# Performance work log

Hardware: AMD Instinct MI355X
Metric: run time of the kernel (lower is better)

Reference implementation:

```python
import jax, jax.numpy as jnp
import numpy as np

B, H, S, D = 2, 12, 2048, 64

def setup_inputs() -> dict:
    key = jax.random.key(0)
    kq, kk, kv = jax.random.split(key, 3)
    Q = jax.random.normal(kq, (B, H, S, D), dtype=jnp.float32)
    K = jax.random.normal(kk, (B, H, S, D), dtype=jnp.float32)
    V = jax.random.normal(kv, (B, H, S, D), dtype=jnp.float32)
    return {"Q": Q, "K": K, "V": V}

def reference(Q, K, V):
    # NOTE: original code scales by sqrt(Q.shape[-2]) (the sequence length),
    # not the head dim — reproduced faithfully.
    scale = 1.0 / np.sqrt(Q.shape[-2]).astype(np.float32)
    scores = jnp.einsum('bhqd,bhkd->bhqk', Q, K) * scale  # [B,H,S,S]
    attn = jax.nn.softmax(scores, axis=-1)
    context = jnp.einsum('bhqk,bhkd->bhqd', attn, V)      # [B,H,S,D]
    # torch .squeeze(-1) only removes the last dim if it is size 1; D=64 so no-op
    return context
```

## Files before the change

kernel.cpp:

```cpp
#include <hip/hip_runtime.h>
#include <hip/hip_bf16.h>
#include <math.h>
#include <stdint.h>

#define BATCH 2
#define NH 12
#define SEQ 2048
#define HD 64
#define TQ 64
#define TK 64
#define NHEADS (BATCH*NH)
#define NIT (SEQ / TK)

typedef short bf16x8 __attribute__((ext_vector_type(8)));
typedef float f32x4 __attribute__((ext_vector_type(4)));
typedef float f32x16 __attribute__((ext_vector_type(16)));
typedef unsigned short us4_t __attribute__((ext_vector_type(4)));
typedef unsigned short us8_t __attribute__((ext_vector_type(8)));

#if __has_builtin(__builtin_amdgcn_exp2f)
#define EXP2F(x) __builtin_amdgcn_exp2f(x)
#else
#define EXP2F(x) exp2f(x)
#endif

static __device__ __forceinline__ unsigned short f2bf(float f) {
    unsigned int u = __float_as_uint(f);
    u += 0x7fffu + ((u >> 16) & 1u);
    return (unsigned short)(u >> 16);
}

static __device__ __forceinline__ unsigned int pack2bf(float a, float b) {
    __hip_bfloat162 v = __float22bfloat162_rn(float2{a, b});
    return *(unsigned int*)&v;
}

static __device__ __forceinline__ void async_cp16(const void* g, void* l) {
    __builtin_amdgcn_global_load_lds(
        (const __attribute__((address_space(1))) void*)g,
        (__attribute__((address_space(3))) void*)(uintptr_t)l,
        16, 0, 0);
}

static __device__ __forceinline__ int tile_off(int r, int c) {
    int rp  = r >> 1;
    int pos = (((r & 1) << 3) | c) ^ (rp & 15);
    return rp * 128 + pos * 8;
}

__global__ __launch_bounds__(256)
void prep_kv(const float* __restrict__ K, const float* __restrict__ V,
             unsigned short* __restrict__ Kb, unsigned short* __restrict__ Vtb) {
    __shared__ unsigned short T[64][66];
    const int bh = blockIdx.x >> 5;
    const int s0 = (blockIdx.x & 31) * 64;
    const int tid = threadIdx.x;
    const size_t off = ((size_t)bh * SEQ + s0) * HD;

    #pragma unroll
    for (int u = 0; u < 4; ++u) {
        int idx = u * 1024 + tid * 4;
        float4 a = *(const float4*)&K[off + idx];
        us4_t r4 = { f2bf(a.x), f2bf(a.y), f2bf(a.z), f2bf(a.w) };
        *(us4_t*)&Kb[off + idx] = r4;
    }
    #pragma unroll
    for (int u = 0; u < 4; ++u) {
        int idx = u * 1024 + tid * 4;
        int r = idx >> 6, col = idx & 63;
        float4 a = *(const float4*)&V[off + idx];
        *(unsigned int*)&T[r][col]     = pack2bf(a.x, a.y);
        *(unsigned int*)&T[r][col + 2] = pack2bf(a.z, a.w);
    }
    __syncthreads();
    unsigned short* Vdst = Vtb + (size_t)bh * HD * SEQ;
    const int g = tid & 7, dd = tid >> 3;
    #pragma unroll
    for (int h = 0; h < 2; ++h) {
        int d = dd + 32 * h;
        us8_t r8;
        #pragma unroll
        for (int j = 0; j < 8; ++j) r8[j] = T[g * 8 + j][d];
        *(us8_t*)&Vdst[(size_t)d * SEQ + s0 + g * 8] = r8;
    }
}

__global__ __launch_bounds__(256)
void fa_main(const float* __restrict__ Q,
             const unsigned short* __restrict__ Kb,
             const unsigned short* __restrict__ Vtb,
             float* __restrict__ O, float qs) {
    const int x  = blockIdx.x & 7;
    const int t  = blockIdx.x >> 3;
    const int bh = x + 8 * (t % 3);
    const int qt = t / 3;
    const int q0 = qt * TQ;

    __shared__ __align__(16) unsigned short KtS[2][4096];
    __shared__ __align__(16) unsigned short VtS[2][4096];
    __shared__ __align__(16) unsigned short Ps[4096];
    __shared__ float Lsum[64];
    __shared__ float Linv[64];

    const int tid  = threadIdx.x;
    const int w    = tid >> 6;
    const int mt   = w >> 1;
    const int nt   = w & 1;
    const int lane = tid & 63;
    const int l31  = lane & 31;
    const int hi   = lane >> 5;

    const float*          Qh = Q   + ((size_t)bh * SEQ + q0) * HD;
    const unsigned short* Kh = Kb  + (size_t)bh * SEQ * HD;
    const unsigned short* Vh = Vtb + (size_t)bh * HD * SEQ;

    int rS[2], cS[2];
    #pragma unroll
    for (int i = 0; i < 2; ++i) {
        int rp = w * 8 + 4 * i + (lane >> 4);
        int lc = (lane & 15) ^ (rp & 15);
        rS[i] = 2 * rp + (lc >> 3);
        cS[i] = lc & 7;
    }
    const int dst0 = (w * 8 + 0) * 128, dst1 = (w * 8 + 4) * 128;
    const size_t kG0 = (size_t)rS[0] * HD  + cS[0] * 8;
    const size_t kG1 = (size_t)rS[1] * HD  + cS[1] * 8;
    const size_t vG0 = (size_t)rS[0] * SEQ + cS[0] * 8;
    const size_t vG1 = (size_t)rS[1] * SEQ + cS[1] * 8;

    async_cp16(Kh + kG0, &KtS[0][dst0]);
    async_cp16(Kh + kG1, &KtS[0][dst1]);
    async_cp16(Vh + vG0, &VtS[0][dst0]);
    async_cp16(Vh + vG1, &VtS[0][dst1]);
    #pragma unroll
    for (int u = 0; u < 4; ++u) {
        int idx = u * 1024 + tid * 4;
        int r = idx >> 6, col = idx & 63;
        float4 a = *(const float4*)&Qh[idx];
        uint2 pk = { pack2bf(a.x * qs, a.y * qs), pack2bf(a.z * qs, a.w * qs) };
        *(uint2*)&Ps[tile_off(r, col >> 3) + (col & 7)] = pk;
    }
    __syncthreads();

    bf16x8 qf[4];
    #pragma unroll
    for (int s = 0; s < 4; ++s)
        qf[s] = *(const bf16x8*)&Ps[tile_off(mt * 32 + l31, s * 2 + hi)];
    __syncthreads();

    const int m = mt * 32 + l31;
    int kOffL[4], vOffL[2][2], pW[4], pR[2];
    #pragma unroll
    for (int s = 0; s < 4; ++s) kOffL[s] = tile_off(nt * 32 + l31, s * 2 + hi);
    #pragma unroll
    for (int dt = 0; dt < 2; ++dt)
        #pragma unroll
        for (int ks = 0; ks < 2; ++ks)
            vOffL[dt][ks] = tile_off(dt * 32 + l31, nt * 4 + ks * 2 + hi);
    #pragma unroll
    for (int g = 0; g < 4; ++g) pW[g] = tile_off(m, nt * 4 + g) + hi * 4;
    #pragma unroll
    for (int ks = 0; ks < 2; ++ks) pR[ks] = tile_off(m, nt * 4 + ks * 2 + hi);

    f32x16 o[2];
    o[0] = (f32x16)(0.f);
    o[1] = (f32x16)(0.f);
    float lsum = 0.f;

    for (int it = 0; it < NIT; ++it) {
        const int cur = it & 1;
        if (it + 1 < NIT) {
            const int nb = cur ^ 1;
            const size_t kv = (size_t)(it + 1) * TK;
            async_cp16(Kh + kv * HD + kG0, &KtS[nb][dst0]);
            async_cp16(Kh + kv * HD + kG1, &KtS[nb][dst1]);
            async_cp16(Vh + kv + vG0,      &VtS[nb][dst0]);
            async_cp16(Vh + kv + vG1,      &VtS[nb][dst1]);
        }
        const unsigned short* Ks = KtS[cur];
        const unsigned short* Vs = VtS[cur];

        f32x16 sc = (f32x16)(0.f);
        #pragma unroll
        for (int s = 0; s < 4; ++s) {
            bf16x8 kf = *(const bf16x8*)&Ks[kOffL[s]];
            sc = __builtin_amdgcn_mfma_f32_32x32x16_bf16(kf, qf[s], sc, 0, 0, 0);
        }

        #pragma unroll
        for (int g = 0; g < 4; ++g) {
            float p0 = EXP2F(sc[4*g+0]);
            float p1 = EXP2F(sc[4*g+1]);
            float p2 = EXP2F(sc[4*g+2]);
            float p3 = EXP2F(sc[4*g+3]);
            lsum += (p0 + p1) + (p2 + p3);
            uint2 pk = { pack2bf(p0, p1), pack2bf(p2, p3) };
            *(uint2*)&Ps[pW[g]] = pk;
        }

        bf16x8 pf0 = *(const bf16x8*)&Ps[pR[0]];
        bf16x8 pf1 = *(const bf16x8*)&Ps[pR[1]];
        #pragma unroll
        for (int dt = 0; dt < 2; ++dt) {
            bf16x8 vf0 = *(const bf16x8*)&Vs[vOffL[dt][0]];
            o[dt] = __builtin_amdgcn_mfma_f32_32x32x16_bf16(pf0, vf0, o[dt], 0, 0, 0);
            bf16x8 vf1 = *(const bf16x8*)&Vs[vOffL[dt][1]];
            o[dt] = __builtin_amdgcn_mfma_f32_32x32x16_bf16(pf1, vf1, o[dt], 0, 0, 0);
        }

        __syncthreads();
    }

    lsum += __shfl_xor(lsum, 32, 64);
    float* ORed = (float*)&KtS[0][0];

    if (nt == 1) {
        if (lane < 32) Lsum[mt * 32 + lane] = lsum;
        #pragma unroll
        for (int dt = 0; dt < 2; ++dt) {
            const int d = dt * 32 + l31;
            #pragma unroll
            for (int g = 0; g < 4; ++g) {
                const int m0 = mt * 32 + 8 * g + 4 * hi;
                const int ph = (m0 >> 2) ^ (d & 15);
                float4 v = { o[dt][4*g+0], o[dt][4*g+1], o[dt][4*g+2], o[dt][4*g+3] };
                *(float4*)&ORed[d * 64 + ph * 4] = v;
            }
        }
    }
    __syncthreads();

    if (nt == 0) {
        float ltot = lsum + Lsum[mt * 32 + l31];
        if (lane < 32) Linv[mt * 32 + lane] = 1.0f / ltot;
        float* Oh = O + ((size_t)bh * SEQ + q0) * HD;
        #pragma unroll
        for (int dt = 0; dt < 2; ++dt) {
            const int d = dt * 32 + l31;
            #pragma unroll
            for (int g = 0; g < 4; ++g) {
                const int m0 = mt * 32 + 8 * g + 4 * hi;
                const int ph = (m0 >> 2) ^ (d & 15);
                float4 part = *(const float4*)&ORed[d * 64 + ph * 4];
                float4 inv4 = *(const float4*)&Linv[m0];
                const float* pp = (const float*)&part;
                const float* ii = (const float*)&inv4;
                #pragma unroll
                for (int j = 0; j < 4; ++j)
                    Oh[(size_t)(m0 + j) * HD + d] = (o[dt][4*g+j] + pp[j]) * ii[j];
            }
        }
    }
}

#define PAD 8
#define LSTR (HD + PAD)

__global__ __launch_bounds__(256)
void fa_fwd_fb(const float* __restrict__ Q, const float* __restrict__ K,
               const float* __restrict__ V, float* __restrict__ O) {
    const int x  = blockIdx.x & 7;
    const int t  = blockIdx.x >> 3;
    const int bh = x + 8 * (t % 3);
    const int qt = t / 3;
    const int q0 = qt * TQ;
    const long base = (long)bh * SEQ * HD;

    __shared__ unsigned short Qs[TQ][LSTR];
    __shared__ unsigned short Ks2[TK][LSTR];
    __shared__ unsigned short Vt[HD][TK + PAD];
    __shared__ unsigned short Ps2[4][16][LSTR];

    const int tid  = threadIdx.x;
    const int wave = tid >> 6;
    const int lane = tid & 63;
    const int col  = lane & 15;
    const int quad = lane >> 4;
    const int m0   = wave * 16;

    #pragma unroll
    for (int i = 0; i < 4; ++i) {
        int idx = tid + 256 * i;
        int row = idx >> 4;
        int c4  = (idx & 15) * 4;
        float4 v = *(const float4*)&Q[base + (long)(q0 + row) * HD + c4];
        ushort4 b = { f2bf(v.x), f2bf(v.y), f2bf(v.z), f2bf(v.w) };
        *(ushort4*)&Qs[row][c4] = b;
    }
    __syncthreads();

    bf16x8 aq0 = *(const bf16x8*)&Qs[m0 + col][quad * 8];
    bf16x8 aq1 = *(const bf16x8*)&Qs[m0 + col][32 + quad * 8];

    f32x4 o0 = {0.f,0.f,0.f,0.f}, o1 = o0, o2 = o0, o3 = o0;
    float l[4] = {0.f, 0.f, 0.f, 0.f};
    const float scale = 0.022097086912079608f;

    for (int kv0 = 0; kv0 < SEQ; kv0 += TK) {
        __syncthreads();
        #pragma unroll
        for (int i = 0; i < 4; ++i) {
            int idx = tid + 256 * i;
            int row = idx >> 4;
            int c4  = (idx & 15) * 4;
            float4 kv = *(const float4*)&K[base + (long)(kv0 + row) * HD + c4];
            ushort4 kb = { f2bf(kv.x), f2bf(kv.y), f2bf(kv.z), f2bf(kv.w) };
            *(ushort4*)&Ks2[row][c4] = kb;
            float4 vv = *(const float4*)&V[base + (long)(kv0 + row) * HD + c4];
            Vt[c4 + 0][row] = f2bf(vv.x);
            Vt[c4 + 1][row] = f2bf(vv.y);
            Vt[c4 + 2][row] = f2bf(vv.z);
            Vt[c4 + 3][row] = f2bf(vv.w);
        }
        __syncthreads();

        f32x4 sc[4];
        #pragma unroll
        for (int n = 0; n < 4; ++n) {
            bf16x8 b0 = *(const bf16x8*)&Ks2[n * 16 + col][quad * 8];
            bf16x8 b1 = *(const bf16x8*)&Ks2[n * 16 + col][32 + quad * 8];
            f32x4 acc = {0.f,0.f,0.f,0.f};
            acc = __builtin_amdgcn_mfma_f32_16x16x32_bf16(aq0, b0, acc, 0, 0, 0);
            acc = __builtin_amdgcn_mfma_f32_16x16x32_bf16(aq1, b1, acc, 0, 0, 0);
            sc[n] = acc;
        }

        float tsum[4] = {0.f, 0.f, 0.f, 0.f};
        #pragma unroll
        for (int n = 0; n < 4; ++n) {
            #pragma unroll
            for (int r = 0; r < 4; ++r) {
                float p = __expf(sc[n][r] * scale);
                tsum[r] += p;
                Ps2[wave][quad * 4 + r][n * 16 + col] = f2bf(p);
            }
        }
        #pragma unroll
        for (int off = 1; off < 16; off <<= 1) {
            #pragma unroll
            for (int r = 0; r < 4; ++r) tsum[r] += __shfl_xor(tsum[r], off, 64);
        }
        #pragma unroll
        for (int r = 0; r < 4; ++r) l[r] += tsum[r];

        bf16x8 ap0 = *(const bf16x8*)&Ps2[wave][col][quad * 8];
        bf16x8 ap1 = *(const bf16x8*)&Ps2[wave][col][32 + quad * 8];
        #pragma unroll
        for (int n = 0; n < 4; ++n) {
            bf16x8 b0 = *(const bf16x8*)&Vt[n * 16 + col][quad * 8];
            bf16x8 b1 = *(const bf16x8*)&Vt[n * 16 + col][32 + quad * 8];
            f32x4* op = (n == 0) ? &o0 : (n == 1) ? &o1 : (n == 2) ? &o2 : &o3;
            *op = __builtin_amdgcn_mfma_f32_16x16x32_bf16(ap0, b0, *op, 0, 0, 0);
            *op = __builtin_amdgcn_mfma_f32_16x16x32_bf16(ap1, b1, *op, 0, 0, 0);
        }
    }

    float inv[4];
    #pragma unroll
    for (int r = 0; r < 4; ++r) inv[r] = 1.0f / l[r];
    #pragma unroll
    for (int r = 0; r < 4; ++r) {
        long row = base + (long)(q0 + m0 + quad * 4 + r) * HD;
        O[row +  0 + col] = o0[r] * inv[r];
        O[row + 16 + col] = o1[r] * inv[r];
        O[row + 32 + col] = o2[r] * inv[r];
        O[row + 48 + col] = o3[r] * inv[r];
    }
}

extern "C" void kernel_launch(void* const* d_in, const int* in_sizes, int n_in,
                              void* d_out, int out_size, void* d_ws, size_t ws_size,
                              hipStream_t stream) {
    const float* Q = (const float*)d_in[0];
    const float* K = (const float*)d_in[1];
    const float* V = (const float*)d_in[2];
    float* O = (float*)d_out;

    const size_t tensorElems = (size_t)NHEADS * SEQ * HD;
    const size_t need = 2 * tensorElems * sizeof(unsigned short);

    if (ws_size >= need) {
        unsigned short* Kb  = (unsigned short*)d_ws;
        unsigned short* Vtb = Kb + tensorElems;
        const float qs = (float)(1.4426950408889634 / sqrt(2048.0));
        prep_kv<<<dim3(NHEADS * (SEQ / 64)), dim3(256), 0, stream>>>(K, V, Kb, Vtb);
        fa_main<<<dim3(NHEADS * (SEQ / TQ)), dim3(256), 0, stream>>>(Q, Kb, Vtb, O, qs);
    } else {
        fa_fwd_fb<<<dim3(NHEADS * (SEQ / TQ)), dim3(256), 0, stream>>>(Q, K, V, O);
    }
}
```

Measured before the change: 125.6 us.

## Split KV across waves with register-resident K/V fragments and LDS reduction

Each wave now owns a 32-key slice of a 128-key block and loads its K and V fragments straight from global memory into registers, prefetching the next block one iteration ahead. This replaces the shared-memory double buffer and the per-iteration block barrier. Every wave computes all 64 query rows, so partial outputs and row sums are combined across the four waves through shared memory at the end. The intent is to remove LDS staging traffic and the barriers from the main loop, at the cost of higher register pressure, a serialized four-step reduction, and less coalesced direct global loads.

```diff
diff --git a/kernel.cpp b/kernel.cpp
--- a/kernel.cpp
+++ b/kernel.cpp
@@ -8,9 +8,9 @@
 #define SEQ 2048
 #define HD 64
 #define TQ 64
-#define TK 64
+#define TKK 128
 #define NHEADS (BATCH*NH)
-#define NIT (SEQ / TK)
+#define NITK (SEQ / TKK)
 
 typedef short bf16x8 __attribute__((ext_vector_type(8)));
 typedef float f32x4 __attribute__((ext_vector_type(4)));
@@ -35,17 +35,15 @@
     return *(unsigned int*)&v;
 }
 
-static __device__ __forceinline__ void async_cp16(const void* g, void* l) {
-    __builtin_amdgcn_global_load_lds(
-        (const __attribute__((address_space(1))) void*)g,
-        (__attribute__((address_space(3))) void*)(uintptr_t)l,
-        16, 0, 0);
-}
-
 static __device__ __forceinline__ int tile_off(int r, int c) {
     int rp  = r >> 1;
     int pos = (((r & 1) << 3) | c) ^ (rp & 15);
     return rp * 128 + pos * 8;
+}
+static __device__ __forceinline__ int poff32(int r, int c) {
+    int rp  = r >> 1;
+    int pos = (((r & 1) << 2) | c) ^ (rp & 7);
+    return rp * 64 + pos * 8;
 }
 
 __global__ __launch_bounds__(256)
@@ -96,16 +94,13 @@
     const int qt = t / 3;
     const int q0 = qt * TQ;
 
-    __shared__ __align__(16) unsigned short KtS[2][4096];
-    __shared__ __align__(16) unsigned short VtS[2][4096];
-    __shared__ __align__(16) unsigned short Ps[4096];
-    __shared__ float Lsum[64];
-    __shared__ float Linv[64];
+    __shared__ __align__(16) unsigned char SHraw[18432];
+    unsigned short* Qst   = (unsigned short*)SHraw;
+    float*          ORed  = (float*)SHraw;
+    float*          Lpart = (float*)(SHraw + 17408);
 
     const int tid  = threadIdx.x;
     const int w    = tid >> 6;
-    const int mt   = w >> 1;
-    const int nt   = w & 1;
     const int lane = tid & 63;
     const int l31  = lane & 31;
     const int hi   = lane >> 5;
@@ -114,142 +109,146 @@
     const unsigned short* Kh = Kb  + (size_t)bh * SEQ * HD;
     const unsigned short* Vh = Vtb + (size_t)bh * HD * SEQ;
 
-    int rS[2], cS[2];
-    #pragma unroll
-    for (int i = 0; i < 2; ++i) {
-        int rp = w * 8 + 4 * i + (lane >> 4);
-        int lc = (lane & 15) ^ (rp & 15);
-        rS[i] = 2 * rp + (lc >> 3);
-        cS[i] = lc & 7;
-    }
-    const int dst0 = (w * 8 + 0) * 128, dst1 = (w * 8 + 4) * 128;
-    const size_t kG0 = (size_t)rS[0] * HD  + cS[0] * 8;
-    const size_t kG1 = (size_t)rS[1] * HD  + cS[1] * 8;
-    const size_t vG0 = (size_t)rS[0] * SEQ + cS[0] * 8;
-    const size_t vG1 = (size_t)rS[1] * SEQ + cS[1] * 8;
-
-    async_cp16(Kh + kG0, &KtS[0][dst0]);
-    async_cp16(Kh + kG1, &KtS[0][dst1]);
-    async_cp16(Vh + vG0, &VtS[0][dst0]);
-    async_cp16(Vh + vG1, &VtS[0][dst1]);
+    const unsigned short* Kq = Kh + (size_t)(w * 32 + l31) * HD + hi * 8;
+    const unsigned short* Vq = Vh + (size_t)l31 * SEQ + w * 32 + hi * 8;
+
+    us8_t kc[4], vc[4];
+    #pragma unroll
+    for (int s = 0; s < 4; ++s) kc[s] = *(const us8_t*)&Kq[s * 16];
+    #pragma unroll
+    for (int dt = 0; dt < 2; ++dt)
+        #pragma unroll
+        for (int ks = 0; ks < 2; ++ks)
+            vc[dt * 2 + ks] = *(const us8_t*)&Vq[(size_t)dt * 32 * SEQ + ks * 16];
+
     #pragma unroll
     for (int u = 0; u < 4; ++u) {
         int idx = u * 1024 + tid * 4;
         int r = idx >> 6, col = idx & 63;
         float4 a = *(const float4*)&Qh[idx];
         uint2 pk = { pack2bf(a.x * qs, a.y * qs), pack2bf(a.z * qs, a.w * qs) };
-        *(uint2*)&Ps[tile_off(r, col >> 3) + (col & 7)] = pk;
-    }
-    __syncthreads();
-
-    bf16x8 qf[4];
-    #pragma unroll
-    for (int s = 0; s < 4; ++s)
-        qf[s] = *(const bf16x8*)&Ps[tile_off(mt * 32 + l31, s * 2 + hi)];
-    __syncthreads();
-
-    const int m = mt * 32 + l31;
-    int kOffL[4], vOffL[2][2], pW[4], pR[2];
-    #pragma unroll
-    for (int s = 0; s < 4; ++s) kOffL[s] = tile_off(nt * 32 + l31, s * 2 + hi);
-    #pragma unroll
-    for (int dt = 0; dt < 2; ++dt)
-        #pragma unroll
-        for (int ks = 0; ks < 2; ++ks)
-            vOffL[dt][ks] = tile_off(dt * 32 + l31, nt * 4 + ks * 2 + hi);
-    #pragma unroll
-    for (int g = 0; g < 4; ++g) pW[g] = tile_off(m, nt * 4 + g) + hi * 4;
-    #pragma unroll
-    for (int ks = 0; ks < 2; ++ks) pR[ks] = tile_off(m, nt * 4 + ks * 2 + hi);
-
-    f32x16 o[2];
-    o[0] = (f32x16)(0.f);
-    o[1] = (f32x16)(0.f);
-    float lsum = 0.f;
-
-    for (int it = 0; it < NIT; ++it) {
-        const int cur = it & 1;
-        if (it + 1 < NIT) {
-            const int nb = cur ^ 1;
-            const size_t kv = (size_t)(it + 1) * TK;
-            async_cp16(Kh + kv * HD + kG0, &KtS[nb][dst0]);
-            async_cp16(Kh + kv * HD + kG1, &KtS[nb][dst1]);
-            async_cp16(Vh + kv + vG0,      &VtS[nb][dst0]);
-            async_cp16(Vh + kv + vG1,      &VtS[nb][dst1]);
-        }
-        const unsigned short* Ks = KtS[cur];
-        const unsigned short* Vs = VtS[cur];
-
-        f32x16 sc = (f32x16)(0.f);
+        *(uint2*)&Qst[tile_off(r, col >> 3) + (col & 7)] = pk;
+    }
+    __syncthreads();
+    bf16x8 qf[2][4];
+    #pragma unroll
+    for (int mt = 0; mt < 2; ++mt)
+        #pragma unroll
+        for (int s = 0; s < 4; ++s)
+            qf[mt][s] = *(const bf16x8*)&Qst[tile_off(mt * 32 + l31, s * 2 + hi)];
+    __syncthreads();
+
+    unsigned short* Psw = (unsigned short*)SHraw + w * 2048;
+
+    int pWo[2][4], pRo[2][2];
+    #pragma unroll
+    for (int mt = 0; mt < 2; ++mt) {
+        #pragma unroll
+        for (int g = 0; g < 4; ++g)  pWo[mt][g]  = poff32(mt * 32 + l31, g) + hi * 4;
+        #pragma unroll
+        for (int ks = 0; ks < 2; ++ks) pRo[mt][ks] = poff32(mt * 32 + l31, ks * 2 + hi);
+    }
+
+    f32x16 o[2][2];
+    o[0][0] = (f32x16)(0.f); o[0][1] = (f32x16)(0.f);
+    o[1][0] = (f32x16)(0.f); o[1][1] = (f32x16)(0.f);
+    float lsum[2] = {0.f, 0.f};
+
+    #pragma unroll 2
+    for (int it = 0; it < NITK; ++it) {
+        us8_t kn[4], vn[4];
+        if (it + 1 < NITK) {
+            const size_t ko = (size_t)(it + 1) * TKK * HD;
+            const size_t vo = (size_t)(it + 1) * TKK;
+            #pragma unroll
+            for (int s = 0; s < 4; ++s) kn[s] = *(const us8_t*)&Kq[ko + s * 16];
+            #pragma unroll
+            for (int dt = 0; dt < 2; ++dt)
+                #pragma unroll
+                for (int ks = 0; ks < 2; ++ks)
+                    vn[dt * 2 + ks] = *(const us8_t*)&Vq[vo + (size_t)dt * 32 * SEQ + ks * 16];
+        }
+
+        f32x16 sc0 = (f32x16)(0.f), sc1 = (f32x16)(0.f);
         #pragma unroll
         for (int s = 0; s < 4; ++s) {
-            bf16x8 kf = *(const bf16x8*)&Ks[kOffL[s]];
-            sc = __builtin_amdgcn_mfma_f32_32x32x16_bf16(kf, qf[s], sc, 0, 0, 0);
-        }
-
-        #pragma unroll
-        for (int g = 0; g < 4; ++g) {
-            float p0 = EXP2F(sc[4*g+0]);
-            float p1 = EXP2F(sc[4*g+1]);
-            float p2 = EXP2F(sc[4*g+2]);
-            float p3 = EXP2F(sc[4*g+3]);
-            lsum += (p0 + p1) + (p2 + p3);
-            uint2 pk = { pack2bf(p0, p1), pack2bf(p2, p3) };
-            *(uint2*)&Ps[pW[g]] = pk;
-        }
-
-        bf16x8 pf0 = *(const bf16x8*)&Ps[pR[0]];
-        bf16x8 pf1 = *(const bf16x8*)&Ps[pR[1]];
-        #pragma unroll
-        for (int dt = 0; dt < 2; ++dt) {
-            bf16x8 vf0 = *(const bf16x8*)&Vs[vOffL[dt][0]];
-            o[dt] = __builtin_amdgcn_mfma_f32_32x32x16_bf16(pf0, vf0, o[dt], 0, 0, 0);
-            bf16x8 vf1 = *(const bf16x8*)&Vs[vOffL[dt][1]];
-            o[dt] = __builtin_amdgcn_mfma_f32_32x32x16_bf16(pf1, vf1, o[dt], 0, 0, 0);
-        }
-
+            bf16x8 kf = (bf16x8)kc[s];
+            sc0 = __builtin_amdgcn_mfma_f32_32x32x16_bf16(kf, qf[0][s], sc0, 0, 0, 0);
+            sc1 = __builtin_amdgcn_mfma_f32_32x32x16_bf16(kf, qf[1][s], sc1, 0, 0, 0);
+        }
+
+        #pragma unroll
+        for (int mt = 0; mt < 2; ++mt) {
+            const f32x16 s = mt ? sc1 : sc0;
+            #pragma unroll
+            for (int g = 0; g < 4; ++g) {
+                float p0 = EXP2F(s[4*g+0]);
+                float p1 = EXP2F(s[4*g+1]);
+                float p2 = EXP2F(s[4*g+2]);
+                float p3 = EXP2F(s[4*g+3]);
+                lsum[mt] += (p0 + p1) + (p2 + p3);
+                uint2 pk = { pack2bf(p0, p1), pack2bf(p2, p3) };
+                *(uint2*)&Psw[pWo[mt][g]] = pk;
+            }
+        }
+
+        bf16x8 pf[2][2];
+        #pragma unroll
+        for (int mt = 0; mt < 2; ++mt)
+            #pragma unroll
+            for (int ks = 0; ks < 2; ++ks)
+                pf[mt][ks] = *(const bf16x8*)&Psw[pRo[mt][ks]];
+        #pragma unroll
+        for (int dt = 0; dt < 2; ++dt)
+            #pragma unroll
+            for (int ks = 0; ks < 2; ++ks) {
+                bf16x8 vf = (bf16x8)vc[dt * 2 + ks];
+                o[0][dt] = __builtin_amdgcn_mfma_f32_32x32x16_bf16(pf[0][ks], vf, o[0][dt], 0, 0, 0);
+                o[1][dt] = __builtin_amdgcn_mfma_f32_32x32x16_bf16(pf[1][ks], vf, o[1][dt], 0, 0, 0);
+            }
+
+        #pragma unroll
+        for (int s = 0; s < 4; ++s) { kc[s] = kn[s]; vc[s] = vn[s]; }
+    }
+
+    #pragma unroll
+    for (int mt = 0; mt < 2; ++mt) lsum[mt] += __shfl_xor(lsum[mt], 32, 64);
+    if (lane < 32) {
+        Lpart[w * 64 + l31]      = lsum[0];
+        Lpart[w * 64 + 32 + l31] = lsum[1];
+    }
+
+    #pragma unroll
+    for (int rr = 0; rr < 4; ++rr) {
         __syncthreads();
-    }
-
-    lsum += __shfl_xor(lsum, 32, 64);
-    float* ORed = (float*)&KtS[0][0];
-
-    if (nt == 1) {
-        if (lane < 32) Lsum[mt * 32 + lane] = lsum;
-        #pragma unroll
-        for (int dt = 0; dt < 2; ++dt) {
-            const int d = dt * 32 + l31;
-            #pragma unroll
-            for (int g = 0; g < 4; ++g) {
-                const int m0 = mt * 32 + 8 * g + 4 * hi;
-                const int ph = (m0 >> 2) ^ (d & 15);
-                float4 v = { o[dt][4*g+0], o[dt][4*g+1], o[dt][4*g+2], o[dt][4*g+3] };
-                *(float4*)&ORed[d * 64 + ph * 4] = v;
-            }
-        }
-    }
-    __syncthreads();
-
-    if (nt == 0) {
-        float ltot = lsum + Lsum[mt * 32 + l31];
-        if (lane < 32) Linv[mt * 32 + lane] = 1.0f / ltot;
-        float* Oh = O + ((size_t)bh * SEQ + q0) * HD;
-        #pragma unroll
-        for (int dt = 0; dt < 2; ++dt) {
-            const int d = dt * 32 + l31;
-            #pragma unroll
-            for (int g = 0; g < 4; ++g) {
-                const int m0 = mt * 32 + 8 * g + 4 * hi;
-                const int ph = (m0 >> 2) ^ (d & 15);
-                float4 part = *(const float4*)&ORed[d * 64 + ph * 4];
-                float4 inv4 = *(const float4*)&Linv[m0];
-                const float* pp = (const float*)&part;
-                const float* ii = (const float*)&inv4;
+        if (w == rr) {
+            #pragma unroll
+            for (int mt = 0; mt < 2; ++mt)
                 #pragma unroll
-                for (int j = 0; j < 4; ++j)
-                    Oh[(size_t)(m0 + j) * HD + d] = (o[dt][4*g+j] + pp[j]) * ii[j];
-            }
-        }
+                for (int dt = 0; dt < 2; ++dt) {
+                    const int d = dt * 32 + l31;
+                    #pragma unroll
+                    for (int g = 0; g < 4; ++g) {
+                        const int m0 = mt * 32 + 8 * g + 4 * hi;
+                        float4 v = { o[mt][dt][4*g+0], o[mt][dt][4*g+1],
+                                     o[mt][dt][4*g+2], o[mt][dt][4*g+3] };
+                        if (rr != 0) {
+                            float4 p = *(const float4*)&ORed[d * 68 + m0];
+                            v.x += p.x; v.y += p.y; v.z += p.z; v.w += p.w;
+                        }
+                        *(float4*)&ORed[d * 68 + m0] = v;
+                    }
+                }
+        }
+    }
+    __syncthreads();
+
+    float* Oh = O + ((size_t)bh * SEQ + q0) * HD;
+    #pragma unroll
+    for (int i = 0; i < 16; ++i) {
+        const int m = w * 16 + i;
+        float ltot = Lpart[m] + Lpart[64 + m] + Lpart[128 + m] + Lpart[192 + m];
+        Oh[(size_t)m * HD + lane] = ORed[lane * 68 + m] * (1.0f / ltot);
     }
 }
 
@@ -267,8 +266,8 @@
     const long base = (long)bh * SEQ * HD;
 
     __shared__ unsigned short Qs[TQ][LSTR];
-    __shared__ unsigned short Ks2[TK][LSTR];
-    __shared__ unsigned short Vt[HD][TK + PAD];
+    __shared__ unsigned short Ks2[64][LSTR];
+    __shared__ unsigned short Vt[HD][64 + PAD];
     __shared__ unsigned short Ps2[4][16][LSTR];
 
     const int tid  = threadIdx.x;
@@ -296,7 +295,7 @@
     float l[4] = {0.f, 0.f, 0.f, 0.f};
     const float scale = 0.022097086912079608f;
 
-    for (int kv0 = 0; kv0 < SEQ; kv0 += TK) {
+    for (int kv0 = 0; kv0 < SEQ; kv0 += 64) {
         __syncthreads();
         #pragma unroll
         for (int i = 0; i < 4; ++i) {
```

Measured after the change: 135.7 us. +8.1%, slower.

## Keep softmax probabilities in registers by permuting V layout, drop P shared buffer

Applied to the files above, without the earlier changes.

The V-transpose prep kernel now writes keys in a permuted order that matches the MFMA accumulator layout. This lets the exponentiated scores be packed straight into bf16 B-operand registers for the PV product, with no round-trip through a shared-memory P tile. Shared memory is merged into one raw buffer with the Q staging reusing a V buffer, occupancy is hinted with launch_bounds(256,4), and V fragments are loaded before the QK MFMAs to hide LDS latency. The risk is that a mismatch between the register layout and the key permutation would silently give wrong results.

```diff
diff --git a/kernel.cpp b/kernel.cpp
--- a/kernel.cpp
+++ b/kernel.cpp
@@ -17,6 +17,7 @@
 typedef float f32x16 __attribute__((ext_vector_type(16)));
 typedef unsigned short us4_t __attribute__((ext_vector_type(4)));
 typedef unsigned short us8_t __attribute__((ext_vector_type(8)));
+typedef unsigned int u32x4 __attribute__((ext_vector_type(4)));
 
 #if __has_builtin(__builtin_amdgcn_exp2f)
 #define EXP2F(x) __builtin_amdgcn_exp2f(x)
@@ -80,12 +81,15 @@
         int d = dd + 32 * h;
         us8_t r8;
         #pragma unroll
-        for (int j = 0; j < 8; ++j) r8[j] = T[g * 8 + j][d];
+        for (int j = 0; j < 8; ++j) {
+            int src = ((g >> 1) << 4) + ((j >> 2) << 3) + ((g & 1) << 2) + (j & 3);
+            r8[j] = T[src][d];
+        }
         *(us8_t*)&Vdst[(size_t)d * SEQ + s0 + g * 8] = r8;
     }
 }
 
-__global__ __launch_bounds__(256)
+__global__ __launch_bounds__(256, 4)
 void fa_main(const float* __restrict__ Q,
              const unsigned short* __restrict__ Kb,
              const unsigned short* __restrict__ Vtb,
@@ -96,11 +100,14 @@
     const int qt = t / 3;
     const int q0 = qt * TQ;
 
-    __shared__ __align__(16) unsigned short KtS[2][4096];
-    __shared__ __align__(16) unsigned short VtS[2][4096];
-    __shared__ __align__(16) unsigned short Ps[4096];
-    __shared__ float Lsum[64];
-    __shared__ float Linv[64];
+    __shared__ __align__(16) unsigned char SH[33280];
+    unsigned short* Ksh0 = (unsigned short*)SH;
+    unsigned short* Ksh1 = (unsigned short*)(SH + 8192);
+    unsigned short* Vsh0 = (unsigned short*)(SH + 16384);
+    unsigned short* Vsh1 = (unsigned short*)(SH + 24576);
+    float* Lsum = (float*)(SH + 32768);
+    float* Linv = (float*)(SH + 33024);
+    float* ORed = (float*)SH;
 
     const int tid  = threadIdx.x;
     const int w    = tid >> 6;
@@ -128,28 +135,27 @@
     const size_t vG0 = (size_t)rS[0] * SEQ + cS[0] * 8;
     const size_t vG1 = (size_t)rS[1] * SEQ + cS[1] * 8;
 
-    async_cp16(Kh + kG0, &KtS[0][dst0]);
-    async_cp16(Kh + kG1, &KtS[0][dst1]);
-    async_cp16(Vh + vG0, &VtS[0][dst0]);
-    async_cp16(Vh + vG1, &VtS[0][dst1]);
+    async_cp16(Kh + kG0, &Ksh0[dst0]);
+    async_cp16(Kh + kG1, &Ksh0[dst1]);
+    async_cp16(Vh + vG0, &Vsh0[dst0]);
+    async_cp16(Vh + vG1, &Vsh0[dst1]);
     #pragma unroll
     for (int u = 0; u < 4; ++u) {
         int idx = u * 1024 + tid * 4;
         int r = idx >> 6, col = idx & 63;
         float4 a = *(const float4*)&Qh[idx];
         uint2 pk = { pack2bf(a.x * qs, a.y * qs), pack2bf(a.z * qs, a.w * qs) };
-        *(uint2*)&Ps[tile_off(r, col >> 3) + (col & 7)] = pk;
+        *(uint2*)&Vsh1[tile_off(r, col >> 3) + (col & 7)] = pk;
     }
     __syncthreads();
 
     bf16x8 qf[4];
     #pragma unroll
     for (int s = 0; s < 4; ++s)
-        qf[s] = *(const bf16x8*)&Ps[tile_off(mt * 32 + l31, s * 2 + hi)];
-    __syncthreads();
-
-    const int m = mt * 32 + l31;
-    int kOffL[4], vOffL[2][2], pW[4], pR[2];
+        qf[s] = *(const bf16x8*)&Vsh1[tile_off(mt * 32 + l31, s * 2 + hi)];
+    __syncthreads();
+
+    int kOffL[4], vOffL[2][2];
     #pragma unroll
     for (int s = 0; s < 4; ++s) kOffL[s] = tile_off(nt * 32 + l31, s * 2 + hi);
     #pragma unroll
@@ -157,28 +163,33 @@
         #pragma unroll
         for (int ks = 0; ks < 2; ++ks)
             vOffL[dt][ks] = tile_off(dt * 32 + l31, nt * 4 + ks * 2 + hi);
-    #pragma unroll
-    for (int g = 0; g < 4; ++g) pW[g] = tile_off(m, nt * 4 + g) + hi * 4;
-    #pragma unroll
-    for (int ks = 0; ks < 2; ++ks) pR[ks] = tile_off(m, nt * 4 + ks * 2 + hi);
 
     f32x16 o[2];
     o[0] = (f32x16)(0.f);
     o[1] = (f32x16)(0.f);
     float lsum = 0.f;
 
+    #pragma unroll 2
     for (int it = 0; it < NIT; ++it) {
         const int cur = it & 1;
         if (it + 1 < NIT) {
-            const int nb = cur ^ 1;
             const size_t kv = (size_t)(it + 1) * TK;
-            async_cp16(Kh + kv * HD + kG0, &KtS[nb][dst0]);
-            async_cp16(Kh + kv * HD + kG1, &KtS[nb][dst1]);
-            async_cp16(Vh + kv + vG0,      &VtS[nb][dst0]);
-            async_cp16(Vh + kv + vG1,      &VtS[nb][dst1]);
-        }
-        const unsigned short* Ks = KtS[cur];
-        const unsigned short* Vs = VtS[cur];
+            unsigned short* Kn = cur ? Ksh0 : Ksh1;
+            unsigned short* Vn = cur ? Vsh0 : Vsh1;
+            async_cp16(Kh + kv * HD + kG0, &Kn[dst0]);
+            async_cp16(Kh + kv * HD + kG1, &Kn[dst1]);
+            async_cp16(Vh + kv + vG0,      &Vn[dst0]);
+            async_cp16(Vh + kv + vG1,      &Vn[dst1]);
+        }
+        const unsigned short* Ks = cur ? Ksh1 : Ksh0;
+        const unsigned short* Vs = cur ? Vsh1 : Vsh0;
+
+        bf16x8 vf[2][2];
+        #pragma unroll
+        for (int dt = 0; dt < 2; ++dt)
+            #pragma unroll
+            for (int ks = 0; ks < 2; ++ks)
+                vf[dt][ks] = *(const bf16x8*)&Vs[vOffL[dt][ks]];
 
         f32x16 sc = (f32x16)(0.f);
         #pragma unroll
@@ -187,32 +198,28 @@
             sc = __builtin_amdgcn_mfma_f32_32x32x16_bf16(kf, qf[s], sc, 0, 0, 0);
         }
 
-        #pragma unroll
-        for (int g = 0; g < 4; ++g) {
-            float p0 = EXP2F(sc[4*g+0]);
-            float p1 = EXP2F(sc[4*g+1]);
-            float p2 = EXP2F(sc[4*g+2]);
-            float p3 = EXP2F(sc[4*g+3]);
-            lsum += (p0 + p1) + (p2 + p3);
-            uint2 pk = { pack2bf(p0, p1), pack2bf(p2, p3) };
-            *(uint2*)&Ps[pW[g]] = pk;
-        }
-
-        bf16x8 pf0 = *(const bf16x8*)&Ps[pR[0]];
-        bf16x8 pf1 = *(const bf16x8*)&Ps[pR[1]];
+        float e[16];
+        #pragma unroll
+        for (int r = 0; r < 16; ++r) e[r] = EXP2F(sc[r]);
+        #pragma unroll
+        for (int r = 0; r < 16; ++r) lsum += e[r];
+        union { u32x4 d; bf16x8 h; } pu0, pu1;
+        pu0.d = (u32x4){ pack2bf(e[0],  e[1]),  pack2bf(e[2],  e[3]),
+                         pack2bf(e[4],  e[5]),  pack2bf(e[6],  e[7]) };
+        pu1.d = (u32x4){ pack2bf(e[8],  e[9]),  pack2bf(e[10], e[11]),
+                         pack2bf(e[12], e[13]), pack2bf(e[14], e[15]) };
+        bf16x8 pf0 = pu0.h, pf1 = pu1.h;
+
         #pragma unroll
         for (int dt = 0; dt < 2; ++dt) {
-            bf16x8 vf0 = *(const bf16x8*)&Vs[vOffL[dt][0]];
-            o[dt] = __builtin_amdgcn_mfma_f32_32x32x16_bf16(pf0, vf0, o[dt], 0, 0, 0);
-            bf16x8 vf1 = *(const bf16x8*)&Vs[vOffL[dt][1]];
-            o[dt] = __builtin_amdgcn_mfma_f32_32x32x16_bf16(pf1, vf1, o[dt], 0, 0, 0);
+            o[dt] = __builtin_amdgcn_mfma_f32_32x32x16_bf16(pf0, vf[dt][0], o[dt], 0, 0, 0);
+            o[dt] = __builtin_amdgcn_mfma_f32_32x32x16_bf16(pf1, vf[dt][1], o[dt], 0, 0, 0);
         }
 
         __syncthreads();
     }
 
     lsum += __shfl_xor(lsum, 32, 64);
-    float* ORed = (float*)&KtS[0][0];
 
     if (nt == 1) {
         if (lane < 32) Lsum[mt * 32 + lane] = lsum;
@@ -267,8 +274,8 @@
     const long base = (long)bh * SEQ * HD;
 
     __shared__ unsigned short Qs[TQ][LSTR];
-    __shared__ unsigned short Ks2[TK][LSTR];
-    __shared__ unsigned short Vt[HD][TK + PAD];
+    __shared__ unsigned short Ks2[64][LSTR];
+    __shared__ unsigned short Vt[HD][64 + PAD];
     __shared__ unsigned short Ps2[4][16][LSTR];
 
     const int tid  = threadIdx.x;
@@ -296,7 +303,7 @@
     float l[4] = {0.f, 0.f, 0.f, 0.f};
     const float scale = 0.022097086912079608f;
 
-    for (int kv0 = 0; kv0 < SEQ; kv0 += TK) {
+    for (int kv0 = 0; kv0 < SEQ; kv0 += 64) {
         __syncthreads();
         #pragma unroll
         for (int i = 0; i < 4; ++i) {
```

New measurement: 117.7 us. -6.3%, faster.
